# Kernel tuning notes

Hardware: AMD Instinct MI355X
Metric: run time of the kernel (lower is better)

## Reference

```python
import jax, jax.numpy as jnp
import numpy as np

TOPK = 8


def setup_inputs() -> dict:
    key = jax.random.key(0)
    k1, k2 = jax.random.split(key)
    tokens, dim, n_experts = 16384, 7168, 256
    x = jax.random.normal(k1, (tokens, dim), dtype=jnp.float32)
    # xavier_uniform-ish scale for router weight
    limit = (6.0 / (n_experts + dim)) ** 0.5
    weight = jax.random.uniform(k2, (n_experts, dim), dtype=jnp.float32,
                                minval=-limit, maxval=limit)
    return {"x": x, "weight": weight}


def reference(x, weight):
    # logits: [tokens, n_experts] = x @ weight.T
    logits = jnp.einsum('td,ed->te', x, weight)
    scores = jax.nn.softmax(logits, axis=-1)
    # torch.topk returns values & indices; gather(scores, 1, indices) == values
    weights, indices = jax.lax.top_k(scores, TOPK)
    return weights, indices
```

## Files before the change

kernel.cpp:

```cpp
#include <hip/hip_runtime.h>
#include <math.h>

#define TOKENS 16384
#define DIM    7168
#define NEXP   256
#define TK     8
#define BM     32
#define BK     32
#define NKT    (DIM / BK)

#define AS_OFF(buf)  ((buf) * 1152)
#define BS_OFF(buf)  (2304 + (buf) * 8320)
#define LDS_BYTES    75776

__global__ __launch_bounds__(256, 2)
void gate_f64(const float* __restrict__ x,
              const float* __restrict__ w,
              float* __restrict__ outw,
              float* __restrict__ outi)
{
    extern __shared__ __align__(16) float smemf[];
    double* lgd = (double*)smemf;

    const int t    = threadIdx.x;
    const int tx   = t & 31;
    const int ty   = t >> 5;
    const int lane = t & 63;
    const int wv   = t >> 6;
    const int tok0 = blockIdx.x * BM;

    const int ldq = t >> 3;
    const int kq  = (t & 7) * 4;

    const float* xp = x + (size_t)(tok0 + ldq) * DIM + kq;
    const float* wp = w + (size_t)ldq * DIM + kq;

    double acc[2][4][4];
    #pragma unroll
    for (int eg = 0; eg < 2; ++eg)
        #pragma unroll
        for (int i = 0; i < 4; ++i)
            #pragma unroll
            for (int j = 0; j < 4; ++j)
                acc[eg][i][j] = 0.0;

    float4 ar, br0, br1, br2, br3, br4, br5, br6, br7;

#define LOADT(kt) do {                                        \
    const float* xq = xp + (size_t)(kt) * BK;                 \
    ar  = *(const float4*)(xq);                               \
    const float* wq = wp + (size_t)(kt) * BK;                 \
    br0 = *(const float4*)(wq);                               \
    br1 = *(const float4*)(wq + (size_t) 32 * DIM);           \
    br2 = *(const float4*)(wq + (size_t) 64 * DIM);           \
    br3 = *(const float4*)(wq + (size_t) 96 * DIM);           \
    br4 = *(const float4*)(wq + (size_t)128 * DIM);           \
    br5 = *(const float4*)(wq + (size_t)160 * DIM);           \
    br6 = *(const float4*)(wq + (size_t)192 * DIM);           \
    br7 = *(const float4*)(wq + (size_t)224 * DIM);           \
} while (0)

#define STB(Bw, i, v)                                         \
    (Bw)[(kq+0)*260 + ldq + (i)*32] = (v).x;                  \
    (Bw)[(kq+1)*260 + ldq + (i)*32] = (v).y;                  \
    (Bw)[(kq+2)*260 + ldq + (i)*32] = (v).z;                  \
    (Bw)[(kq+3)*260 + ldq + (i)*32] = (v).w;

#define STASH(buf) do {                                       \
    float* Aw = smemf + AS_OFF(buf);                          \
    Aw[(kq+0)*36 + ldq] = ar.x;                               \
    Aw[(kq+1)*36 + ldq] = ar.y;                               \
    Aw[(kq+2)*36 + ldq] = ar.z;                               \
    Aw[(kq+3)*36 + ldq] = ar.w;                               \
    float* Bw = smemf + BS_OFF(buf);                          \
    STB(Bw, 0, br0) STB(Bw, 1, br1) STB(Bw, 2, br2)           \
    STB(Bw, 3, br3) STB(Bw, 4, br4) STB(Bw, 5, br5)           \
    STB(Bw, 6, br6) STB(Bw, 7, br7)                           \
} while (0)

    LOADT(0);
    STASH(0);
    __syncthreads();

    for (int kt = 0; kt < NKT; ++kt) {
        const int cur = kt & 1;
        if (kt + 1 < NKT) LOADT(kt + 1);
        const float* Ac = smemf + AS_OFF(cur);
        const float* Bc = smemf + BS_OFF(cur);
        #pragma unroll 16
        for (int kk = 0; kk < BK; ++kk) {
            float4 a4 = *(const float4*)(Ac + kk * 36 + ty * 4);
            float4 b0 = *(const float4*)(Bc + kk * 260 + tx * 4);
            float4 b1 = *(const float4*)(Bc + kk * 260 + tx * 4 + 128);
            double ad[4], bd0[4], bd1[4];
            ad[0]  = a4.x; ad[1]  = a4.y; ad[2]  = a4.z; ad[3]  = a4.w;
            bd0[0] = b0.x; bd0[1] = b0.y; bd0[2] = b0.z; bd0[3] = b0.w;
            bd1[0] = b1.x; bd1[1] = b1.y; bd1[2] = b1.z; bd1[3] = b1.w;
            #pragma unroll
            for (int i = 0; i < 4; ++i)
                #pragma unroll
                for (int j = 0; j < 4; ++j) {
                    acc[0][i][j] = fma(ad[i], bd0[j], acc[0][i][j]);
                    acc[1][i][j] = fma(ad[i], bd1[j], acc[1][i][j]);
                }
        }
        if (kt + 1 < NKT) STASH((kt + 1) & 1);
        __syncthreads();
    }

    #pragma unroll
    for (int i = 0; i < 4; ++i) {
        double* lr = lgd + (size_t)(ty * 4 + i) * NEXP + tx * 4;
        lr[0]   = acc[0][i][0]; lr[1]   = acc[0][i][1];
        lr[2]   = acc[0][i][2]; lr[3]   = acc[0][i][3];
        lr[128] = acc[1][i][0]; lr[129] = acc[1][i][1];
        lr[130] = acc[1][i][2]; lr[131] = acc[1][i][3];
    }
    __syncthreads();

    for (int r8 = 0; r8 < 8; ++r8) {
        const int row  = wv * 8 + r8;
        const int gtok = tok0 + row;
        const double* lr = lgd + (size_t)row * NEXP + lane * 4;
        double vv[4];
        vv[0] = lr[0]; vv[1] = lr[1]; vv[2] = lr[2]; vv[3] = lr[3];

        double m = fmax(fmax(vv[0], vv[1]), fmax(vv[2], vv[3]));
        #pragma unroll
        for (int off = 32; off >= 1; off >>= 1)
            m = fmax(m, __shfl_xor(m, off));

        float s = expf((float)(vv[0] - m)) + expf((float)(vv[1] - m))
                + expf((float)(vv[2] - m)) + expf((float)(vv[3] - m));
        #pragma unroll
        for (int off = 32; off >= 1; off >>= 1)
            s += __shfl_xor(s, off);
        const float invs = 1.0f / s;

        int taken = 0;
        for (int it = 0; it < TK; ++it) {
            double bv = -1.0e300;
            int    bi = 1 << 30;
            #pragma unroll
            for (int j = 0; j < 4; ++j) {
                double cv = ((taken >> j) & 1) ? -1.0e300 : vv[j];
                int    ci = lane * 4 + j;
                if (cv > bv || (cv == bv && ci < bi)) { bv = cv; bi = ci; }
            }
            #pragma unroll
            for (int off = 32; off >= 1; off >>= 1) {
                double ov = __shfl_xor(bv, off);
                int    oi = __shfl_xor(bi, off);
                if (ov > bv || (ov == bv && oi < bi)) { bv = ov; bi = oi; }
            }
            if (lane == it) {
                outw[(size_t)gtok * TK + it] = expf((float)(bv - m)) * invs;
                outi[(size_t)gtok * TK + it] = (float)bi;
            }
            if ((bi >> 2) == lane) taken |= 1 << (bi & 3);
        }
    }
}

extern "C" void kernel_launch(void* const* d_in, const int* in_sizes, int n_in,
                              void* d_out, int out_size, void* d_ws, size_t ws_size,
                              hipStream_t stream) {
    const float* x = (const float*)d_in[0];
    const float* w = (const float*)d_in[1];
    float* outw = (float*)d_out;
    float* outi = outw + (size_t)TOKENS * TK;
    gate_f64<<<dim3(TOKENS / BM), dim3(256), LDS_BYTES, stream>>>(x, w, outw, outi);
}
```

Before: 1.499 ms.

## Compute logits in fp32 and recompute near-boundary top-k candidates in fp64

The main GEMM moves from fp64 FMAs to fp32 FMAs, so the bulk of the arithmetic runs at single-precision rate. To keep the top-k selection robust, each token gathers up to 16 candidates whose fp32 logit lies within a fixed delta of the 8th largest. It recomputes those dot products in fp64 from global memory and reselects the top 8 from them. LDS strides are also padded for fewer bank conflicts. The fixed delta may not cover every fp32 rounding gap, and the per-candidate rescoring adds global reads.

```diff
diff --git a/kernel.cpp b/kernel.cpp
--- a/kernel.cpp
+++ b/kernel.cpp
@@ -8,19 +8,21 @@
 #define BM     32
 #define BK     32
 #define NKT    (DIM / BK)
-
-#define AS_OFF(buf)  ((buf) * 1152)
-#define BS_OFF(buf)  (2304 + (buf) * 8320)
-#define LDS_BYTES    75776
+#define DELTA  8.0e-3f
+
+#define AS_OFF(buf)  ((buf) * (32 * 37))
+#define BS_OFF(buf)  (2 * 32 * 37 + (buf) * (32 * 261))
+#define LDS_FLOATS   (2 * 32 * 37 + 2 * 32 * 261)
+#define LDS_BYTES    (LDS_FLOATS * 4)
 
 __global__ __launch_bounds__(256, 2)
-void gate_f64(const float* __restrict__ x,
-              const float* __restrict__ w,
-              float* __restrict__ outw,
-              float* __restrict__ outi)
+void gate_f32r(const float* __restrict__ x,
+               const float* __restrict__ w,
+               float* __restrict__ outw,
+               float* __restrict__ outi)
 {
     extern __shared__ __align__(16) float smemf[];
-    double* lgd = (double*)smemf;
+    float* lgf = smemf;
 
     const int t    = threadIdx.x;
     const int tx   = t & 31;
@@ -35,14 +37,14 @@
     const float* xp = x + (size_t)(tok0 + ldq) * DIM + kq;
     const float* wp = w + (size_t)ldq * DIM + kq;
 
-    double acc[2][4][4];
+    float acc[2][4][4];
     #pragma unroll
     for (int eg = 0; eg < 2; ++eg)
         #pragma unroll
         for (int i = 0; i < 4; ++i)
             #pragma unroll
             for (int j = 0; j < 4; ++j)
-                acc[eg][i][j] = 0.0;
+                acc[eg][i][j] = 0.0f;
 
     float4 ar, br0, br1, br2, br3, br4, br5, br6, br7;
 
@@ -61,17 +63,17 @@
 } while (0)
 
 #define STB(Bw, i, v)                                         \
-    (Bw)[(kq+0)*260 + ldq + (i)*32] = (v).x;                  \
-    (Bw)[(kq+1)*260 + ldq + (i)*32] = (v).y;                  \
-    (Bw)[(kq+2)*260 + ldq + (i)*32] = (v).z;                  \
-    (Bw)[(kq+3)*260 + ldq + (i)*32] = (v).w;
+    (Bw)[(kq+0)*261 + ldq + (i)*32] = (v).x;                  \
+    (Bw)[(kq+1)*261 + ldq + (i)*32] = (v).y;                  \
+    (Bw)[(kq+2)*261 + ldq + (i)*32] = (v).z;                  \
+    (Bw)[(kq+3)*261 + ldq + (i)*32] = (v).w;
 
 #define STASH(buf) do {                                       \
     float* Aw = smemf + AS_OFF(buf);                          \
-    Aw[(kq+0)*36 + ldq] = ar.x;                               \
-    Aw[(kq+1)*36 + ldq] = ar.y;                               \
-    Aw[(kq+2)*36 + ldq] = ar.z;                               \
-    Aw[(kq+3)*36 + ldq] = ar.w;                               \
+    Aw[(kq+0)*37 + ldq] = ar.x;                               \
+    Aw[(kq+1)*37 + ldq] = ar.y;                               \
+    Aw[(kq+2)*37 + ldq] = ar.z;                               \
+    Aw[(kq+3)*37 + ldq] = ar.w;                               \
     float* Bw = smemf + BS_OFF(buf);                          \
     STB(Bw, 0, br0) STB(Bw, 1, br1) STB(Bw, 2, br2)           \
     STB(Bw, 3, br3) STB(Bw, 4, br4) STB(Bw, 5, br5)           \
@@ -89,19 +91,19 @@
         const float* Bc = smemf + BS_OFF(cur);
         #pragma unroll 16
         for (int kk = 0; kk < BK; ++kk) {
-            float4 a4 = *(const float4*)(Ac + kk * 36 + ty * 4);
-            float4 b0 = *(const float4*)(Bc + kk * 260 + tx * 4);
-            float4 b1 = *(const float4*)(Bc + kk * 260 + tx * 4 + 128);
-            double ad[4], bd0[4], bd1[4];
-            ad[0]  = a4.x; ad[1]  = a4.y; ad[2]  = a4.z; ad[3]  = a4.w;
-            bd0[0] = b0.x; bd0[1] = b0.y; bd0[2] = b0.z; bd0[3] = b0.w;
-            bd1[0] = b1.x; bd1[1] = b1.y; bd1[2] = b1.z; bd1[3] = b1.w;
+            float4 a4 = *(const float4*)(Ac + kk * 37 + ty * 4);
+            float4 b0 = *(const float4*)(Bc + kk * 261 + tx * 4);
+            float4 b1 = *(const float4*)(Bc + kk * 261 + tx * 4 + 128);
+            float af[4], b0f[4], b1f[4];
+            af[0]=a4.x; af[1]=a4.y; af[2]=a4.z; af[3]=a4.w;
+            b0f[0]=b0.x; b0f[1]=b0.y; b0f[2]=b0.z; b0f[3]=b0.w;
+            b1f[0]=b1.x; b1f[1]=b1.y; b1f[2]=b1.z; b1f[3]=b1.w;
             #pragma unroll
             for (int i = 0; i < 4; ++i)
                 #pragma unroll
                 for (int j = 0; j < 4; ++j) {
-                    acc[0][i][j] = fma(ad[i], bd0[j], acc[0][i][j]);
-                    acc[1][i][j] = fma(ad[i], bd1[j], acc[1][i][j]);
+                    acc[0][i][j] = fmaf(af[i], b0f[j], acc[0][i][j]);
+                    acc[1][i][j] = fmaf(af[i], b1f[j], acc[1][i][j]);
                 }
         }
         if (kt + 1 < NKT) STASH((kt + 1) & 1);
@@ -110,54 +112,102 @@
 
     #pragma unroll
     for (int i = 0; i < 4; ++i) {
-        double* lr = lgd + (size_t)(ty * 4 + i) * NEXP + tx * 4;
-        lr[0]   = acc[0][i][0]; lr[1]   = acc[0][i][1];
-        lr[2]   = acc[0][i][2]; lr[3]   = acc[0][i][3];
-        lr[128] = acc[1][i][0]; lr[129] = acc[1][i][1];
-        lr[130] = acc[1][i][2]; lr[131] = acc[1][i][3];
+        float* lr = lgf + (size_t)(ty * 4 + i) * 260 + tx * 4;
+        float4 v0, v1;
+        v0.x = acc[0][i][0]; v0.y = acc[0][i][1];
+        v0.z = acc[0][i][2]; v0.w = acc[0][i][3];
+        v1.x = acc[1][i][0]; v1.y = acc[1][i][1];
+        v1.z = acc[1][i][2]; v1.w = acc[1][i][3];
+        *(float4*)(lr)       = v0;
+        *(float4*)(lr + 128) = v1;
     }
     __syncthreads();
 
     for (int r8 = 0; r8 < 8; ++r8) {
         const int row  = wv * 8 + r8;
         const int gtok = tok0 + row;
-        const double* lr = lgd + (size_t)row * NEXP + lane * 4;
-        double vv[4];
-        vv[0] = lr[0]; vv[1] = lr[1]; vv[2] = lr[2]; vv[3] = lr[3];
-
-        double m = fmax(fmax(vv[0], vv[1]), fmax(vv[2], vv[3]));
+        float4 v = *(const float4*)(lgf + (size_t)row * 260 + lane * 4);
+        float vv[4] = {v.x, v.y, v.z, v.w};
+
+        float m = fmaxf(fmaxf(vv[0], vv[1]), fmaxf(vv[2], vv[3]));
         #pragma unroll
         for (int off = 32; off >= 1; off >>= 1)
-            m = fmax(m, __shfl_xor(m, off));
-
-        float s = expf((float)(vv[0] - m)) + expf((float)(vv[1] - m))
-                + expf((float)(vv[2] - m)) + expf((float)(vv[3] - m));
+            m = fmaxf(m, __shfl_xor(m, off));
+
+        float s = expf(vv[0] - m) + expf(vv[1] - m)
+                + expf(vv[2] - m) + expf(vv[3] - m);
         #pragma unroll
         for (int off = 32; off >= 1; off >>= 1)
             s += __shfl_xor(s, off);
         const float invs = 1.0f / s;
 
-        int taken = 0;
+        int   taken = 0;
+        int   ncand = 0;
+        float s8    = 0.0f;
+        float my_cv = -INFINITY;
+        int   my_ci = 1 << 30;
+        for (int it = 0; it < 16; ++it) {
+            float bv = -INFINITY;
+            int   bi = 1 << 30;
+            #pragma unroll
+            for (int j = 0; j < 4; ++j) {
+                float cv = ((taken >> j) & 1) ? -INFINITY : vv[j];
+                int   ci = lane * 4 + j;
+                if (cv > bv || (cv == bv && ci < bi)) { bv = cv; bi = ci; }
+            }
+            #pragma unroll
+            for (int off = 32; off >= 1; off >>= 1) {
+                float ov = __shfl_xor(bv, off);
+                int   oi = __shfl_xor(bi, off);
+                if (ov > bv || (ov == bv && oi < bi)) { bv = ov; bi = oi; }
+            }
+            if (it == 7) s8 = bv;
+            if (it >= 8 && bv < s8 - DELTA) break;
+            if (lane == it) { my_cv = bv; my_ci = bi; }
+            if ((bi >> 2) == lane) taken |= 1 << (bi & 3);
+            ncand = it + 1;
+        }
+        (void)my_cv;
+
+        double ev = -1.0e300;
+        const float* xrow = x + (size_t)gtok * DIM;
+        for (int c = 0; c < ncand; ++c) {
+            const int e = __shfl(my_ci, c);
+            const float* wrow = w + (size_t)e * DIM;
+            double a2 = 0.0;
+            #pragma unroll 4
+            for (int j = 0; j < 28; ++j) {
+                float4 xa = *(const float4*)(xrow + j * 256 + lane * 4);
+                float4 wa = *(const float4*)(wrow + j * 256 + lane * 4);
+                a2 = fma((double)xa.x, (double)wa.x, a2);
+                a2 = fma((double)xa.y, (double)wa.y, a2);
+                a2 = fma((double)xa.z, (double)wa.z, a2);
+                a2 = fma((double)xa.w, (double)wa.w, a2);
+            }
+            #pragma unroll
+            for (int off = 32; off >= 1; off >>= 1)
+                a2 += __shfl_xor(a2, off);
+            if (lane == c) ev = a2;
+        }
+
         for (int it = 0; it < TK; ++it) {
-            double bv = -1.0e300;
-            int    bi = 1 << 30;
-            #pragma unroll
-            for (int j = 0; j < 4; ++j) {
-                double cv = ((taken >> j) & 1) ? -1.0e300 : vv[j];
-                int    ci = lane * 4 + j;
-                if (cv > bv || (cv == bv && ci < bi)) { bv = cv; bi = ci; }
-            }
+            double bv2 = ev;
+            int    bi2 = my_ci;
+            int    bs2 = lane;
             #pragma unroll
             for (int off = 32; off >= 1; off >>= 1) {
-                double ov = __shfl_xor(bv, off);
-                int    oi = __shfl_xor(bi, off);
-                if (ov > bv || (ov == bv && oi < bi)) { bv = ov; bi = oi; }
+                double ov = __shfl_xor(bv2, off);
+                int    oi = __shfl_xor(bi2, off);
+                int    os = __shfl_xor(bs2, off);
+                if (ov > bv2 || (ov == bv2 && oi < bi2)) {
+                    bv2 = ov; bi2 = oi; bs2 = os;
+                }
             }
             if (lane == it) {
-                outw[(size_t)gtok * TK + it] = expf((float)(bv - m)) * invs;
-                outi[(size_t)gtok * TK + it] = (float)bi;
-            }
-            if ((bi >> 2) == lane) taken |= 1 << (bi & 3);
+                outw[(size_t)gtok * TK + it] = expf((float)bv2 - m) * invs;
+                outi[(size_t)gtok * TK + it] = (float)bi2;
+            }
+            if (lane == bs2) ev = -1.0e300;
         }
     }
 }
@@ -169,5 +219,5 @@
     const float* w = (const float*)d_in[1];
     float* outw = (float*)d_out;
     float* outi = outw + (size_t)TOKENS * TK;
-    gate_f64<<<dim3(TOKENS / BM), dim3(256), LDS_BYTES, stream>>>(x, w, outw, outi);
+    gate_f32r<<<dim3(TOKENS / BM), dim3(256), LDS_BYTES, stream>>>(x, w, outw, outi);
 }
```

After: 4.338 ms. 189% more time.
